# Performance work log

Measured on AMD Instinct MI355X. Metric: run time of the kernel, lower is better.

## Reference

```python
import jax, jax.numpy as jnp
import numpy as np

N_NODES = 32768
N_EDGES = 524288
IN_F = 256
OUT_F = 128
NB = 4


def setup_inputs() -> dict:
    key = jax.random.key(0)
    ks = jax.random.split(key, 12)
    s_in = 1.0 / np.sqrt(IN_F)
    s_out = 1.0 / np.sqrt(OUT_F)
    s_cat = 1.0 / np.sqrt(OUT_F * NB)
    return {
        "x": jax.random.normal(ks[0], (N_NODES, IN_F), dtype=jnp.float32),
        "edge_index": jax.random.randint(ks[1], (2, N_EDGES), 0, N_NODES, dtype=jnp.int64),
        "Wb": jax.random.uniform(ks[2], (NB, IN_F, OUT_F), jnp.float32, -s_in, s_in),
        "bb": jax.random.uniform(ks[3], (NB, OUT_F), jnp.float32, -s_in, s_in),
        "W1": jax.random.uniform(ks[4], (NB, OUT_F, OUT_F), jnp.float32, -s_out, s_out),
        "b1": jax.random.uniform(ks[5], (NB, OUT_F), jnp.float32, -s_out, s_out),
        "W2": jax.random.uniform(ks[6], (NB, OUT_F, OUT_F), jnp.float32, -s_out, s_out),
        "b2": jax.random.uniform(ks[7], (NB, OUT_F), jnp.float32, -s_out, s_out),
        "branch_gates": jnp.ones((NB,), dtype=jnp.float32),
        "temperature": jnp.asarray(1.0, dtype=jnp.float32),
        "Wo": jax.random.uniform(ks[8], (OUT_F * NB, OUT_F), jnp.float32, -s_cat, s_cat),
        "bo": jax.random.uniform(ks[9], (OUT_F,), jnp.float32, -s_cat, s_cat),
    }


def _scatter_mean_step(h, row, col, inv_deg):
    # gather per-edge source features, mean-reduce onto destination nodes
    sums = jax.ops.segment_sum(h[row], col, num_segments=N_NODES)
    return sums * inv_deg


def reference(x, edge_index, Wb, bb, W1, b1, W2, b2, branch_gates, temperature, Wo, bo):
    row, col = edge_index[0], edge_index[1]
    deg = jax.ops.segment_sum(jnp.ones((N_EDGES,), x.dtype), col, num_segments=N_NODES)
    inv_deg = (1.0 / jnp.maximum(deg, 1.0))[:, None]  # empty segments -> 0 (scatter_mean semantics)

    gates = jax.nn.softmax(branch_gates / temperature)

    branch_outputs = []
    for i in range(NB):
        h = x @ Wb[i] + bb[i]                   # [N, OUT_F]
        for _ in range(i):                       # scale = scales[i % 4] = i
            h = _scatter_mean_step(h, row, col, inv_deg)
        h = jax.nn.relu(h @ W1[i] + b1[i]) @ W2[i] + b2[i]
        branch_outputs.append(h * gates[i])

    concat = jnp.concatenate(branch_outputs, axis=1)  # [N, NB*OUT_F]
    return concat @ Wo + bo
```

## Files before the change

### kernel.cpp

```cpp
#include <hip/hip_runtime.h>
#include <math.h>

#define N_NODES 32768
#define N_EDGES 524288
#define IN_F    256
#define OUT_F   128
#define NB      4
#define STRIDE  96

#define NE_BLK   256
#define CONV_BLK 1024
#define GX_BLK   2048
#define GEMM_BLK (N_NODES / 128)
#define M_BLK    (N_NODES / 256)

typedef __attribute__((ext_vector_type(8))) short bf16x8;
typedef __attribute__((ext_vector_type(4))) float f32x4;

__device__ __forceinline__ ushort f2b(float f) {
    uint u = __float_as_uint(f);
    return (ushort)((u + 0x7fffu + ((u >> 16) & 1u)) >> 16);
}
__device__ __forceinline__ float b2f_lo(uint v) { return __uint_as_float(v << 16); }
__device__ __forceinline__ float b2f_hi(uint v) { return __uint_as_float(v & 0xffff0000u); }

__device__ __forceinline__ float softmax_gate(const float* bg, const float* temp, int i) {
    float T = temp[0];
    float mx = fmaxf(fmaxf(bg[0], bg[1]), fmaxf(bg[2], bg[3]));
    float e0 = expf((bg[0] - mx) / T), e1 = expf((bg[1] - mx) / T);
    float e2 = expf((bg[2] - mx) / T), e3 = expf((bg[3] - mx) / T);
    float s = e0 + e1 + e2 + e3;
    float ei = (i == 0) ? e0 : (i == 1) ? e1 : (i == 2) ? e2 : e3;
    return ei / s;
}

__device__ __forceinline__ int detect_i32(const int* __restrict__ ei, int* sflag) {
    if (threadIdx.x < 64) {
        unsigned long long b = __ballot(ei[2 * threadIdx.x + 1] != 0);
        if (threadIdx.x == 0) *sflag = (b != 0ull) ? 1 : 0;
    }
    __syncthreads();
    return *sflag;
}

__global__ __launch_bounds__(256) void fill_all_kernel(
    const int* __restrict__ ei, int* __restrict__ cursor, int* __restrict__ srcs,
    const float* __restrict__ x, ushort* __restrict__ xb,
    const float* __restrict__ Wb, const float* __restrict__ W1,
    const float* __restrict__ W2, const float* __restrict__ Wo,
    const float* __restrict__ bb, const float* __restrict__ b2,
    const float* __restrict__ bo, const float* __restrict__ bg,
    const float* __restrict__ temp,
    ushort* __restrict__ WcT, ushort* __restrict__ WzT,
    float* __restrict__ u, float* __restrict__ cvec) {
    __shared__ float smem[16 * 128];
    __shared__ int sflag;
    int b = blockIdx.x;
    int tid = threadIdx.x;
    if (b < NE_BLK) {
        int i32 = detect_i32(ei, &sflag);
#pragma unroll
        for (int it = 0; it < 8; it++) {
            int e = b * 2048 + it * 256 + tid;
            int r, c;
            if (i32 == 0) { r = ei[2 * e]; c = ei[2 * (N_EDGES + e)]; }
            else          { r = ei[e];     c = ei[N_EDGES + e]; }
            int slot = atomicAdd(&cursor[c], 1);
            if (slot < STRIDE) srcs[(size_t)c * STRIDE + slot] = r;
        }
        return;
    }
    b -= NE_BLK;
    if (b < CONV_BLK) {
#pragma unroll
        for (int it = 0; it < 8; it++) {
            int idx = b * 2048 + it * 256 + tid;
            float4 v = ((const float4*)x)[idx];
            ushort4 o;
            o.x = f2b(v.x); o.y = f2b(v.y); o.z = f2b(v.z); o.w = f2b(v.w);
            ((ushort4*)xb)[idx] = o;
        }
        return;
    }
    b -= CONV_BLK;
    int f = tid & 127, rh = tid >> 7;
    if (b < 64) {
        int i = b >> 4, k0 = (b & 15) * 16;
#pragma unroll
        for (int rr = 0; rr < 8; rr++)
            smem[(rh * 8 + rr) * 128 + f] = Wb[((size_t)i * IN_F + k0 + rh * 8 + rr) * OUT_F + f];
        __syncthreads();
        float acc[8] = {};
        const float* W1i = W1 + (size_t)i * OUT_F * OUT_F;
        for (int j = 0; j < OUT_F; j++) {
            float w1 = W1i[j * OUT_F + f];
#pragma unroll
            for (int rr = 0; rr < 8; rr++) acc[rr] += smem[(rh * 8 + rr) * 128 + j] * w1;
        }
        ushort tmp[8];
#pragma unroll
        for (int rr = 0; rr < 8; rr++) tmp[rr] = f2b(acc[rr]);
        *(uint4*)(WcT + ((size_t)i * OUT_F + f) * IN_F + k0 + rh * 8) = *(uint4*)tmp;
    } else if (b < 96) {
        int id = b - 64;
        int i = id >> 3, j0 = (id & 7) * 16;
#pragma unroll
        for (int rr = 0; rr < 8; rr++)
            smem[(rh * 8 + rr) * 128 + f] = W2[((size_t)i * OUT_F + j0 + rh * 8 + rr) * OUT_F + f];
        __syncthreads();
        float acc[8] = {};
        for (int l = 0; l < OUT_F; l++) {
            float wo = Wo[((size_t)i * OUT_F + l) * OUT_F + f];
#pragma unroll
            for (int rr = 0; rr < 8; rr++) acc[rr] += smem[(rh * 8 + rr) * 128 + l] * wo;
        }
        float g = softmax_gate(bg, temp, i);
        ushort tmp[8];
#pragma unroll
        for (int rr = 0; rr < 8; rr++) tmp[rr] = f2b(g * acc[rr]);
        *(uint4*)(WzT + (size_t)f * (NB * OUT_F) + i * OUT_F + j0 + rh * 8) = *(uint4*)tmp;
    } else {
        int id = b - 96;
        int jc = rh;
        if (id < NB) {
            int i = id;
            float partial = 0.f;
            for (int j = jc * 64; j < jc * 64 + 64; j++)
                partial += bb[i * OUT_F + j] * W1[((size_t)i * OUT_F + j) * OUT_F + f];
            smem[jc * 128 + f] = partial;
            __syncthreads();
            if (jc == 0) u[i * OUT_F + f] = smem[f] + smem[128 + f];
        } else {
            int i = id - NB;
            float partial = 0.f;
            for (int j = jc * 64; j < jc * 64 + 64; j++)
                partial += b2[i * OUT_F + j] * Wo[((size_t)i * OUT_F + j) * OUT_F + f];
            smem[jc * 128 + f] = partial;
            __syncthreads();
            if (jc == 0) {
                float tot = (smem[f] + smem[128 + f]) * softmax_gate(bg, temp, i);
                if (i == 0) tot += bo[f];
                atomicAdd(&cvec[f], tot);
            }
        }
    }
}

#define ACC8(A, V)                                                              \
    A[0] += b2f_lo(V.x); A[1] += b2f_hi(V.x);                                   \
    A[2] += b2f_lo(V.y); A[3] += b2f_hi(V.y);                                   \
    A[4] += b2f_lo(V.z); A[5] += b2f_hi(V.z);                                   \
    A[6] += b2f_lo(V.w); A[7] += b2f_hi(V.w)

#define GATHER_256(INBUF)                                                       \
    float a0[8] = {0.f,0.f,0.f,0.f,0.f,0.f,0.f,0.f};                            \
    float a1[8] = {0.f,0.f,0.f,0.f,0.f,0.f,0.f,0.f};                            \
    int p = s;                                                                  \
    for (; p + 8 <= e; p += 8) {                                                \
        int base = p + 4 * half;                                                \
        int2 s01 = *(const int2*)(srcs + base);                                 \
        int2 s23 = *(const int2*)(srcs + base + 2);                             \
        uint4 v0 = *(const uint4*)(INBUF + (size_t)s01.x * IN_F + fl * 8);      \
        uint4 v1 = *(const uint4*)(INBUF + (size_t)s01.y * IN_F + fl * 8);      \
        uint4 v2 = *(const uint4*)(INBUF + (size_t)s23.x * IN_F + fl * 8);      \
        uint4 v3 = *(const uint4*)(INBUF + (size_t)s23.y * IN_F + fl * 8);      \
        ACC8(a0, v0); ACC8(a1, v1); ACC8(a0, v2); ACC8(a1, v3);                 \
    }                                                                           \
    for (; p + 4 <= e; p += 4) {                                                \
        int2 ss = *(const int2*)(srcs + p + 2 * half);                          \
        uint4 v0 = *(const uint4*)(INBUF + (size_t)ss.x * IN_F + fl * 8);       \
        uint4 v1 = *(const uint4*)(INBUF + (size_t)ss.y * IN_F + fl * 8);       \
        ACC8(a0, v0); ACC8(a1, v1);                                             \
    }                                                                           \
    for (; p + half < e; p += 2) {                                              \
        int src = srcs[p + half];                                               \
        uint4 v0 = *(const uint4*)(INBUF + (size_t)src * IN_F + fl * 8);        \
        ACC8(a0, v0);                                                           \
    }                                                                           \
    _Pragma("unroll") for (int k = 0; k < 8; k++) a0[k] += a1[k];               \
    _Pragma("unroll") for (int k = 0; k < 8; k++) a0[k] += __shfl_down(a0[k], 32);

__global__ __launch_bounds__(256) void prop_x_kernel(
    const ushort* __restrict__ xb, ushort* __restrict__ X1b,
    const int* __restrict__ deg, float* __restrict__ m2,
    const int* __restrict__ srcs) {
    int blk = blockIdx.x;
    int tid = threadIdx.x;
    if (blk >= GX_BLK) {
        int n = (blk - GX_BLK) * 256 + tid;
        int d = deg[n];
        int s = n * STRIDE, e = s + ((d < STRIDE) ? d : STRIDE);
        float sum = 0.f;
        for (int p = s; p < e; ++p) sum += (deg[srcs[p]] > 0) ? 1.0f : 0.0f;
        m2[n] = sum / (float)((d > 1) ? d : 1);
        return;
    }
    int lane = tid & 63;
    int half = lane >> 5, fl = lane & 31;
    for (int i = 0; i < 4; i++) {
        int node = blk * 16 + i * 4 + (tid >> 6);
        int d = deg[node];
        int s = node * STRIDE, e = s + ((d < STRIDE) ? d : STRIDE);
        GATHER_256(xb);
        if (half == 0) {
            float w = 1.0f / (float)((d > 1) ? d : 1);
            uint4 o;
            o.x = (uint)f2b(a0[0] * w) | ((uint)f2b(a0[1] * w) << 16);
            o.y = (uint)f2b(a0[2] * w) | ((uint)f2b(a0[3] * w) << 16);
            o.z = (uint)f2b(a0[4] * w) | ((uint)f2b(a0[5] * w) << 16);
            o.w = (uint)f2b(a0[6] * w) | ((uint)f2b(a0[7] * w) << 16);
            *(uint4*)(X1b + (size_t)node * IN_F + fl * 8) = o;
        }
    }
}

__global__ __launch_bounds__(256) void gemmP_kernel(
    const ushort* __restrict__ xb, const ushort* __restrict__ X1b,
    const ushort* __restrict__ WcT, const float* __restrict__ u,
    const float* __restrict__ b1, const int* __restrict__ deg,
    ushort* __restrict__ R, ushort* __restrict__ PQ) {
    int y = blockIdx.y;
    const ushort* A = (y == 0) ? xb : X1b;
    const ushort* WT = WcT + (size_t)y * OUT_F * IN_F;
    int m0 = blockIdx.x * 128;
    __shared__ ushort As[128][72];
    __shared__ ushort Bs[128][72];
    int tid = threadIdx.x;
    int wv = tid >> 6, lane = tid & 63, quad = lane >> 4, lm = lane & 15;
    f32x4 acc[2][8];
    f32x4 zero = {0.f, 0.f, 0.f, 0.f};
#pragma unroll
    for (int i = 0; i < 2; i++)
#pragma unroll
        for (int j = 0; j < 8; j++) acc[i][j] = zero;
    for (int k0 = 0; k0 < IN_F; k0 += 64) {
        __syncthreads();
#pragma unroll
        for (int it = 0; it < 4; it++) {
            int c = tid + 256 * it;
            int r = c >> 3, c8 = c & 7;
            *(uint4*)&As[r][c8 * 8] = *(const uint4*)(A + (size_t)(m0 + r) * IN_F + k0 + c8 * 8);
            *(uint4*)&Bs[r][c8 * 8] = *(const uint4*)(WT + (size_t)r * IN_F + k0 + c8 * 8);
        }
        __syncthreads();
#pragma unroll
        for (int ks = 0; ks < 2; ks++) {
            bf16x8 af0 = *(const bf16x8*)&As[wv * 32 + lm][ks * 32 + quad * 8];
            bf16x8 af1 = *(const bf16x8*)&As[wv * 32 + 16 + lm][ks * 32 + quad * 8];
#pragma unroll
            for (int nt = 0; nt < 8; nt++) {
                bf16x8 bf = *(const bf16x8*)&Bs[nt * 16 + lm][ks * 32 + quad * 8];
                acc[0][nt] = __builtin_amdgcn_mfma_f32_16x16x32_bf16(af0, bf, acc[0][nt], 0, 0, 0);
                acc[1][nt] = __builtin_amdgcn_mfma_f32_16x16x32_bf16(af1, bf, acc[1][nt], 0, 0, 0);
            }
        }
    }
    if (y >= 2) {
        int pqoff = (y - 2) * OUT_F;
#pragma unroll
        for (int mt = 0; mt < 2; mt++)
#pragma unroll
            for (int r = 0; r < 4; r++) {
                int row = m0 + wv * 32 + mt * 16 + quad * 4 + r;
#pragma unroll
                for (int nt = 0; nt < 8; nt++) {
                    int col = nt * 16 + lm;
                    PQ[(size_t)row * IN_F + pqoff + col] = f2b(acc[mt][nt][r]);
                }
            }
    } else {
        float uv[8], bv[8];
#pragma unroll
        for (int nt = 0; nt < 8; nt++) {
            int col = nt * 16 + lm;
            uv[nt] = u[y * OUT_F + col];
            bv[nt] = b1[y * OUT_F + col];
        }
#pragma unroll
        for (int mt = 0; mt < 2; mt++)
#pragma unroll
            for (int r = 0; r < 4; r++) {
                int row = m0 + wv * 32 + mt * 16 + quad * 4 + r;
                float mval = (y == 0) ? 1.0f : ((deg[row] > 0) ? 1.0f : 0.0f);
#pragma unroll
                for (int nt = 0; nt < 8; nt++) {
                    int col = nt * 16 + lm;
                    float h = acc[mt][nt][r] + mval * uv[nt] + bv[nt];
                    R[(size_t)row * (NB * OUT_F) + y * OUT_F + col] = f2b(fmaxf(h, 0.f));
                }
            }
    }
}

__global__ __launch_bounds__(256) void prop_pq_kernel(
    const ushort* __restrict__ PQ, ushort* __restrict__ R, ushort* __restrict__ Qp,
    const int* __restrict__ deg, const float* __restrict__ m2, float* __restrict__ m3,
    const float* __restrict__ u2, const float* __restrict__ b12,
    const int* __restrict__ srcs) {
    int blk = blockIdx.x;
    int tid = threadIdx.x;
    if (blk >= GX_BLK) {
        int n = (blk - GX_BLK) * 256 + tid;
        int d = deg[n];
        int s = n * STRIDE, e = s + ((d < STRIDE) ? d : STRIDE);
        float sum = 0.f;
        for (int p = s; p < e; ++p) sum += m2[srcs[p]];
        m3[n] = sum / (float)((d > 1) ? d : 1);
        return;
    }
    int lane = tid & 63;
    int half = lane >> 5, fl = lane & 31;
    for (int i = 0; i < 4; i++) {
        int node = blk * 16 + i * 4 + (tid >> 6);
        int d = deg[node];
        int s = node * STRIDE, e = s + ((d < STRIDE) ? d : STRIDE);
        GATHER_256(PQ);
        if (half == 0) {
            float w = 1.0f / (float)((d > 1) ? d : 1);
            if (fl < 16) {
                int col = fl * 8;
                float mv = m2[node];
                float4 ua = *(const float4*)(u2 + col);
                float4 ub = *(const float4*)(u2 + col + 4);
                float4 ba = *(const float4*)(b12 + col);
                float4 bb_ = *(const float4*)(b12 + col + 4);
                float o_[8];
                o_[0] = fmaxf(a0[0] * w + mv * ua.x + ba.x, 0.f);
                o_[1] = fmaxf(a0[1] * w + mv * ua.y + ba.y, 0.f);
                o_[2] = fmaxf(a0[2] * w + mv * ua.z + ba.z, 0.f);
                o_[3] = fmaxf(a0[3] * w + mv * ua.w + ba.w, 0.f);
                o_[4] = fmaxf(a0[4] * w + mv * ub.x + bb_.x, 0.f);
                o_[5] = fmaxf(a0[5] * w + mv * ub.y + bb_.y, 0.f);
                o_[6] = fmaxf(a0[6] * w + mv * ub.z + bb_.z, 0.f);
                o_[7] = fmaxf(a0[7] * w + mv * ub.w + bb_.w, 0.f);
                uint4 o;
                o.x = (uint)f2b(o_[0]) | ((uint)f2b(o_[1]) << 16);
                o.y = (uint)f2b(o_[2]) | ((uint)f2b(o_[3]) << 16);
                o.z = (uint)f2b(o_[4]) | ((uint)f2b(o_[5]) << 16);
                o.w = (uint)f2b(o_[6]) | ((uint)f2b(o_[7]) << 16);
                *(uint4*)(R + (size_t)node * (NB * OUT_F) + 2 * OUT_F + col) = o;
            } else {
                int col = (fl - 16) * 8;
                uint4 o;
                o.x = (uint)f2b(a0[0] * w) | ((uint)f2b(a0[1] * w) << 16);
                o.y = (uint)f2b(a0[2] * w) | ((uint)f2b(a0[3] * w) << 16);
                o.z = (uint)f2b(a0[4] * w) | ((uint)f2b(a0[5] * w) << 16);
                o.w = (uint)f2b(a0[6] * w) | ((uint)f2b(a0[7] * w) << 16);
                *(uint4*)(Qp + (size_t)node * OUT_F + col) = o;
            }
        }
    }
}

__global__ __launch_bounds__(256) void prop_q_kernel(
    const ushort* __restrict__ Qp, ushort* __restrict__ R,
    const int* __restrict__ deg, const float* __restrict__ m3,
    const float* __restrict__ u3, const float* __restrict__ b13,
    const int* __restrict__ srcs) {
    int lane = threadIdx.x & 63;
    int q = lane >> 4, fl = lane & 15;
    for (int i = 0; i < 4; i++) {
        int node = blockIdx.x * 16 + i * 4 + (threadIdx.x >> 6);
        int d = deg[node];
        int s = node * STRIDE, e = s + ((d < STRIDE) ? d : STRIDE);
        float a[8] = {0.f,0.f,0.f,0.f,0.f,0.f,0.f,0.f};
        float b[8] = {0.f,0.f,0.f,0.f,0.f,0.f,0.f,0.f};
        int p = s;
        for (; p + 8 <= e; p += 8) {
            int2 ss = *(const int2*)(srcs + p + 2 * q);
            uint4 v0 = *(const uint4*)(Qp + (size_t)ss.x * OUT_F + fl * 8);
            uint4 v1 = *(const uint4*)(Qp + (size_t)ss.y * OUT_F + fl * 8);
            ACC8(a, v0); ACC8(b, v1);
        }
        for (; p + 4 <= e; p += 4) {
            int src = srcs[p + q];
            uint4 v0 = *(const uint4*)(Qp + (size_t)src * OUT_F + fl * 8);
            ACC8(a, v0);
        }
        if (p + q < e) {
            int src = srcs[p + q];
            uint4 v0 = *(const uint4*)(Qp + (size_t)src * OUT_F + fl * 8);
            ACC8(a, v0);
        }
#pragma unroll
        for (int k = 0; k < 8; k++) a[k] += b[k];
#pragma unroll
        for (int k = 0; k < 8; k++) a[k] += __shfl_down(a[k], 32);
#pragma unroll
        for (int k = 0; k < 8; k++) a[k] += __shfl_down(a[k], 16);
        if (lane < 16) {
            float w = 1.0f / (float)((d > 1) ? d : 1);
            float mv = m3[node];
            int col = fl * 8;
            float4 ua = *(const float4*)(u3 + col);
            float4 ub = *(const float4*)(u3 + col + 4);
            float4 ba = *(const float4*)(b13 + col);
            float4 bb_ = *(const float4*)(b13 + col + 4);
            float o_[8];
            o_[0] = fmaxf(a[0] * w + mv * ua.x + ba.x, 0.f);
            o_[1] = fmaxf(a[1] * w + mv * ua.y + ba.y, 0.f);
            o_[2] = fmaxf(a[2] * w + mv * ua.z + ba.z, 0.f);
            o_[3] = fmaxf(a[3] * w + mv * ua.w + ba.w, 0.f);
            o_[4] = fmaxf(a[4] * w + mv * ub.x + bb_.x, 0.f);
            o_[5] = fmaxf(a[5] * w + mv * ub.y + bb_.y, 0.f);
            o_[6] = fmaxf(a[6] * w + mv * ub.z + bb_.z, 0.f);
            o_[7] = fmaxf(a[7] * w + mv * ub.w + bb_.w, 0.f);
            uint4 o;
            o.x = (uint)f2b(o_[0]) | ((uint)f2b(o_[1]) << 16);
            o.y = (uint)f2b(o_[2]) | ((uint)f2b(o_[3]) << 16);
            o.z = (uint)f2b(o_[4]) | ((uint)f2b(o_[5]) << 16);
            o.w = (uint)f2b(o_[6]) | ((uint)f2b(o_[7]) << 16);
            *(uint4*)(R + (size_t)node * (NB * OUT_F) + 3 * OUT_F + col) = o;
        }
    }
}

__global__ __launch_bounds__(256) void gemm2_mfma_kernel(
    const ushort* __restrict__ R, const ushort* __restrict__ WzT,
    const float* __restrict__ cvec, float* __restrict__ out) {
    int m0 = blockIdx.x * 128;
    const int K = NB * OUT_F;
    __shared__ ushort As[128][72];
    __shared__ ushort Bs[128][72];
    int tid = threadIdx.x;
    int wv = tid >> 6, lane = tid & 63, quad = lane >> 4, lm = lane & 15;
    f32x4 acc[2][8];
    f32x4 zero = {0.f, 0.f, 0.f, 0.f};
#pragma unroll
    for (int i = 0; i < 2; i++)
#pragma unroll
        for (int j = 0; j < 8; j++) acc[i][j] = zero;
    for (int k0 = 0; k0 < K; k0 += 64) {
        __syncthreads();
#pragma unroll
        for (int it = 0; it < 4; it++) {
            int c = tid + 256 * it;
            int r = c >> 3, c8 = c & 7;
            *(uint4*)&As[r][c8 * 8] = *(const uint4*)(R + (size_t)(m0 + r) * K + k0 + c8 * 8);
            *(uint4*)&Bs[r][c8 * 8] = *(const uint4*)(WzT + (size_t)r * K + k0 + c8 * 8);
        }
        __syncthreads();
#pragma unroll
        for (int ks = 0; ks < 2; ks++) {
            bf16x8 af0 = *(const bf16x8*)&As[wv * 32 + lm][ks * 32 + quad * 8];
            bf16x8 af1 = *(const bf16x8*)&As[wv * 32 + 16 + lm][ks * 32 + quad * 8];
#pragma unroll
            for (int nt = 0; nt < 8; nt++) {
                bf16x8 bf = *(const bf16x8*)&Bs[nt * 16 + lm][ks * 32 + quad * 8];
                acc[0][nt] = __builtin_amdgcn_mfma_f32_16x16x32_bf16(af0, bf, acc[0][nt], 0, 0, 0);
                acc[1][nt] = __builtin_amdgcn_mfma_f32_16x16x32_bf16(af1, bf, acc[1][nt], 0, 0, 0);
            }
        }
    }
    float cb[8];
#pragma unroll
    for (int nt = 0; nt < 8; nt++) cb[nt] = cvec[nt * 16 + lm];
#pragma unroll
    for (int mt = 0; mt < 2; mt++)
#pragma unroll
        for (int r = 0; r < 4; r++) {
            int row = m0 + wv * 32 + mt * 16 + quad * 4 + r;
#pragma unroll
            for (int nt = 0; nt < 8; nt++) {
                int col = nt * 16 + lm;
                out[(size_t)row * OUT_F + col] = acc[mt][nt][r] + cb[nt];
            }
        }
}

extern "C" void kernel_launch(void* const* d_in, const int* in_sizes, int n_in,
                              void* d_out, int out_size, void* d_ws, size_t ws_size,
                              hipStream_t stream) {
    const float* x    = (const float*)d_in[0];
    const int*   ei   = (const int*)d_in[1];
    const float* Wb   = (const float*)d_in[2];
    const float* bb   = (const float*)d_in[3];
    const float* W1   = (const float*)d_in[4];
    const float* b1   = (const float*)d_in[5];
    const float* W2   = (const float*)d_in[6];
    const float* b2   = (const float*)d_in[7];
    const float* bg   = (const float*)d_in[8];
    const float* temp = (const float*)d_in[9];
    const float* Wo   = (const float*)d_in[10];
    const float* bo   = (const float*)d_in[11];
    float* out = (float*)d_out;

    char* w = (char*)d_ws;
    size_t used = 0;
    auto alloc = [&](size_t bytes) {
        char* p = w + used;
        used += (bytes + 255) & ~(size_t)255;
        return p;
    };
    int*    cursor = (int*)alloc(N_NODES * 4);
    float*  cvec   = (float*)alloc(OUT_F * 4);
    int*    srcs   = (int*)alloc((size_t)N_NODES * STRIDE * 4);
    float*  m2v    = (float*)alloc(N_NODES * 4);
    float*  m3v    = (float*)alloc(N_NODES * 4);
    float*  u      = (float*)alloc(NB * OUT_F * 4);
    ushort* WcT    = (ushort*)alloc((size_t)NB * IN_F * OUT_F * 2);
    ushort* WzT    = (ushort*)alloc((size_t)NB * OUT_F * OUT_F * 2);
    ushort* xb     = (ushort*)alloc((size_t)N_NODES * IN_F * 2);
    ushort* X1b    = (ushort*)alloc((size_t)N_NODES * IN_F * 2);
    ushort* PQ     = (ushort*)alloc((size_t)N_NODES * IN_F * 2);
    ushort* Qp     = (ushort*)alloc((size_t)N_NODES * OUT_F * 2);
    ushort* R      = (ushort*)alloc((size_t)N_NODES * NB * OUT_F * 2);
    if (used > ws_size) return;

    int* deg = cursor;

    hipMemsetAsync(cursor, 0, N_NODES * 4 + 512, stream);

    fill_all_kernel<<<NE_BLK + CONV_BLK + 104, 256, 0, stream>>>(
        ei, cursor, srcs, x, xb, Wb, W1, W2, Wo, bb, b2, bo, bg, temp, WcT, WzT, u, cvec);

    prop_x_kernel<<<GX_BLK + M_BLK, 256, 0, stream>>>(xb, X1b, deg, m2v, srcs);

    {
        dim3 grid(GEMM_BLK, 4);
        gemmP_kernel<<<grid, 256, 0, stream>>>(xb, X1b, WcT, u, b1, deg, R, PQ);
    }

    prop_pq_kernel<<<GX_BLK + M_BLK, 256, 0, stream>>>(
        PQ, R, Qp, deg, m2v, m3v, u + 2 * OUT_F, b1 + 2 * OUT_F, srcs);

    prop_q_kernel<<<GX_BLK, 256, 0, stream>>>(
        Qp, R, deg, m3v, u + 3 * OUT_F, b1 + 3 * OUT_F, srcs);

    gemm2_mfma_kernel<<<GEMM_BLK, 256, 0, stream>>>(R, WzT, cvec, out);
}
```

Before: 269.2 us.

## Use nontemporal loads/stores, deepen gather unrolling, reorder blocks, add occupancy hints

Switches edge-index loads, the srcs/xb/X1b/PQ/R/Qp/out writes, and the srcs index reads to nontemporal builtins so streaming data bypasses the cache. The gather loops are unrolled further (12 edges per iteration in GATHER_256, 16 in prop_q) to put more loads in flight. The per-node m2/m3 blocks are moved to the front of the grid, and launch_bounds min-blocks hints of 8 are added to the propagation kernels. The risk is that nontemporal stores push out data the following kernel reads straight back (xb, PQ, Qp, R), and that the occupancy hint caps registers and causes spills.

New measurement: 303.8 us. 1.13x slower.

```diff
diff --git a/kernel.cpp b/kernel.cpp
--- a/kernel.cpp
+++ b/kernel.cpp
@@ -16,6 +16,10 @@
 
 typedef __attribute__((ext_vector_type(8))) short bf16x8;
 typedef __attribute__((ext_vector_type(4))) float f32x4;
+typedef __attribute__((ext_vector_type(2))) int    i32x2;
+typedef __attribute__((ext_vector_type(4))) int    i32x4;
+typedef __attribute__((ext_vector_type(4))) uint   u32x4;
+typedef __attribute__((ext_vector_type(4))) ushort u16x4;
 
 __device__ __forceinline__ ushort f2b(float f) {
     uint u = __float_as_uint(f);
@@ -63,10 +67,15 @@
         for (int it = 0; it < 8; it++) {
             int e = b * 2048 + it * 256 + tid;
             int r, c;
-            if (i32 == 0) { r = ei[2 * e]; c = ei[2 * (N_EDGES + e)]; }
-            else          { r = ei[e];     c = ei[N_EDGES + e]; }
+            if (i32 == 0) {
+                r = __builtin_nontemporal_load(ei + 2 * e);
+                c = __builtin_nontemporal_load(ei + 2 * (N_EDGES + e));
+            } else {
+                r = __builtin_nontemporal_load(ei + e);
+                c = __builtin_nontemporal_load(ei + N_EDGES + e);
+            }
             int slot = atomicAdd(&cursor[c], 1);
-            if (slot < STRIDE) srcs[(size_t)c * STRIDE + slot] = r;
+            if (slot < STRIDE) __builtin_nontemporal_store(r, srcs + (size_t)c * STRIDE + slot);
         }
         return;
     }
@@ -75,10 +84,10 @@
 #pragma unroll
         for (int it = 0; it < 8; it++) {
             int idx = b * 2048 + it * 256 + tid;
-            float4 v = ((const float4*)x)[idx];
-            ushort4 o;
+            f32x4 v = __builtin_nontemporal_load((const f32x4*)x + idx);
+            u16x4 o;
             o.x = f2b(v.x); o.y = f2b(v.y); o.z = f2b(v.z); o.w = f2b(v.w);
-            ((ushort4*)xb)[idx] = o;
+            __builtin_nontemporal_store(o, (u16x4*)xb + idx);
         }
         return;
     }
@@ -156,18 +165,22 @@
     float a0[8] = {0.f,0.f,0.f,0.f,0.f,0.f,0.f,0.f};                            \
     float a1[8] = {0.f,0.f,0.f,0.f,0.f,0.f,0.f,0.f};                            \
     int p = s;                                                                  \
-    for (; p + 8 <= e; p += 8) {                                                \
-        int base = p + 4 * half;                                                \
-        int2 s01 = *(const int2*)(srcs + base);                                 \
-        int2 s23 = *(const int2*)(srcs + base + 2);                             \
+    for (; p + 12 <= e; p += 12) {                                              \
+        int base = p + 6 * half;                                                \
+        i32x2 s01 = __builtin_nontemporal_load((const i32x2*)(srcs + base));    \
+        i32x2 s23 = __builtin_nontemporal_load((const i32x2*)(srcs + base + 2));\
+        i32x2 s45 = __builtin_nontemporal_load((const i32x2*)(srcs + base + 4));\
         uint4 v0 = *(const uint4*)(INBUF + (size_t)s01.x * IN_F + fl * 8);      \
         uint4 v1 = *(const uint4*)(INBUF + (size_t)s01.y * IN_F + fl * 8);      \
         uint4 v2 = *(const uint4*)(INBUF + (size_t)s23.x * IN_F + fl * 8);      \
         uint4 v3 = *(const uint4*)(INBUF + (size_t)s23.y * IN_F + fl * 8);      \
-        ACC8(a0, v0); ACC8(a1, v1); ACC8(a0, v2); ACC8(a1, v3);                 \
+        uint4 v4 = *(const uint4*)(INBUF + (size_t)s45.x * IN_F + fl * 8);      \
+        uint4 v5 = *(const uint4*)(INBUF + (size_t)s45.y * IN_F + fl * 8);      \
+        ACC8(a0, v0); ACC8(a1, v1); ACC8(a0, v2);                               \
+        ACC8(a1, v3); ACC8(a0, v4); ACC8(a1, v5);                               \
     }                                                                           \
     for (; p + 4 <= e; p += 4) {                                                \
-        int2 ss = *(const int2*)(srcs + p + 2 * half);                          \
+        i32x2 ss = __builtin_nontemporal_load((const i32x2*)(srcs + p + 2 * half)); \
         uint4 v0 = *(const uint4*)(INBUF + (size_t)ss.x * IN_F + fl * 8);       \
         uint4 v1 = *(const uint4*)(INBUF + (size_t)ss.y * IN_F + fl * 8);       \
         ACC8(a0, v0); ACC8(a1, v1);                                             \
@@ -180,14 +193,14 @@
     _Pragma("unroll") for (int k = 0; k < 8; k++) a0[k] += a1[k];               \
     _Pragma("unroll") for (int k = 0; k < 8; k++) a0[k] += __shfl_down(a0[k], 32);
 
-__global__ __launch_bounds__(256) void prop_x_kernel(
+__global__ __launch_bounds__(256, 8) void prop_x_kernel(
     const ushort* __restrict__ xb, ushort* __restrict__ X1b,
     const int* __restrict__ deg, float* __restrict__ m2,
     const int* __restrict__ srcs) {
     int blk = blockIdx.x;
     int tid = threadIdx.x;
-    if (blk >= GX_BLK) {
-        int n = (blk - GX_BLK) * 256 + tid;
+    if (blk < M_BLK) {
+        int n = blk * 256 + tid;
         int d = deg[n];
         int s = n * STRIDE, e = s + ((d < STRIDE) ? d : STRIDE);
         float sum = 0.f;
@@ -195,6 +208,7 @@
         m2[n] = sum / (float)((d > 1) ? d : 1);
         return;
     }
+    blk -= M_BLK;
     int lane = tid & 63;
     int half = lane >> 5, fl = lane & 31;
     for (int i = 0; i < 4; i++) {
@@ -204,12 +218,12 @@
         GATHER_256(xb);
         if (half == 0) {
             float w = 1.0f / (float)((d > 1) ? d : 1);
-            uint4 o;
+            u32x4 o;
             o.x = (uint)f2b(a0[0] * w) | ((uint)f2b(a0[1] * w) << 16);
             o.y = (uint)f2b(a0[2] * w) | ((uint)f2b(a0[3] * w) << 16);
             o.z = (uint)f2b(a0[4] * w) | ((uint)f2b(a0[5] * w) << 16);
             o.w = (uint)f2b(a0[6] * w) | ((uint)f2b(a0[7] * w) << 16);
-            *(uint4*)(X1b + (size_t)node * IN_F + fl * 8) = o;
+            __builtin_nontemporal_store(o, (u32x4*)(X1b + (size_t)node * IN_F + fl * 8));
         }
     }
 }
@@ -265,7 +279,8 @@
 #pragma unroll
                 for (int nt = 0; nt < 8; nt++) {
                     int col = nt * 16 + lm;
-                    PQ[(size_t)row * IN_F + pqoff + col] = f2b(acc[mt][nt][r]);
+                    __builtin_nontemporal_store(f2b(acc[mt][nt][r]),
+                                                PQ + (size_t)row * IN_F + pqoff + col);
                 }
             }
     } else {
@@ -286,21 +301,22 @@
                 for (int nt = 0; nt < 8; nt++) {
                     int col = nt * 16 + lm;
                     float h = acc[mt][nt][r] + mval * uv[nt] + bv[nt];
-                    R[(size_t)row * (NB * OUT_F) + y * OUT_F + col] = f2b(fmaxf(h, 0.f));
+                    __builtin_nontemporal_store(f2b(fmaxf(h, 0.f)),
+                                                R + (size_t)row * (NB * OUT_F) + y * OUT_F + col);
                 }
             }
     }
 }
 
-__global__ __launch_bounds__(256) void prop_pq_kernel(
+__global__ __launch_bounds__(256, 8) void prop_pq_kernel(
     const ushort* __restrict__ PQ, ushort* __restrict__ R, ushort* __restrict__ Qp,
     const int* __restrict__ deg, const float* __restrict__ m2, float* __restrict__ m3,
     const float* __restrict__ u2, const float* __restrict__ b12,
     const int* __restrict__ srcs) {
     int blk = blockIdx.x;
     int tid = threadIdx.x;
-    if (blk >= GX_BLK) {
-        int n = (blk - GX_BLK) * 256 + tid;
+    if (blk < M_BLK) {
+        int n = blk * 256 + tid;
         int d = deg[n];
         int s = n * STRIDE, e = s + ((d < STRIDE) ? d : STRIDE);
         float sum = 0.f;
@@ -308,6 +324,7 @@
         m3[n] = sum / (float)((d > 1) ? d : 1);
         return;
     }
+    blk -= M_BLK;
     int lane = tid & 63;
     int half = lane >> 5, fl = lane & 31;
     for (int i = 0; i < 4; i++) {
@@ -333,26 +350,26 @@
                 o_[5] = fmaxf(a0[5] * w + mv * ub.y + bb_.y, 0.f);
                 o_[6] = fmaxf(a0[6] * w + mv * ub.z + bb_.z, 0.f);
                 o_[7] = fmaxf(a0[7] * w + mv * ub.w + bb_.w, 0.f);
-                uint4 o;
+                u32x4 o;
                 o.x = (uint)f2b(o_[0]) | ((uint)f2b(o_[1]) << 16);
                 o.y = (uint)f2b(o_[2]) | ((uint)f2b(o_[3]) << 16);
                 o.z = (uint)f2b(o_[4]) | ((uint)f2b(o_[5]) << 16);
                 o.w = (uint)f2b(o_[6]) | ((uint)f2b(o_[7]) << 16);
-                *(uint4*)(R + (size_t)node * (NB * OUT_F) + 2 * OUT_F + col) = o;
+                __builtin_nontemporal_store(o, (u32x4*)(R + (size_t)node * (NB * OUT_F) + 2 * OUT_F + col));
             } else {
                 int col = (fl - 16) * 8;
-                uint4 o;
+                u32x4 o;
                 o.x = (uint)f2b(a0[0] * w) | ((uint)f2b(a0[1] * w) << 16);
                 o.y = (uint)f2b(a0[2] * w) | ((uint)f2b(a0[3] * w) << 16);
                 o.z = (uint)f2b(a0[4] * w) | ((uint)f2b(a0[5] * w) << 16);
                 o.w = (uint)f2b(a0[6] * w) | ((uint)f2b(a0[7] * w) << 16);
-                *(uint4*)(Qp + (size_t)node * OUT_F + col) = o;
-            }
-        }
-    }
-}
-
-__global__ __launch_bounds__(256) void prop_q_kernel(
+                __builtin_nontemporal_store(o, (u32x4*)(Qp + (size_t)node * OUT_F + col));
+            }
+        }
+    }
+}
+
+__global__ __launch_bounds__(256, 8) void prop_q_kernel(
     const ushort* __restrict__ Qp, ushort* __restrict__ R,
     const int* __restrict__ deg, const float* __restrict__ m3,
     const float* __restrict__ u3, const float* __restrict__ b13,
@@ -366,8 +383,16 @@
         float a[8] = {0.f,0.f,0.f,0.f,0.f,0.f,0.f,0.f};
         float b[8] = {0.f,0.f,0.f,0.f,0.f,0.f,0.f,0.f};
         int p = s;
+        for (; p + 16 <= e; p += 16) {
+            i32x4 sq = __builtin_nontemporal_load((const i32x4*)(srcs + p + 4 * q));
+            uint4 v0 = *(const uint4*)(Qp + (size_t)sq.x * OUT_F + fl * 8);
+            uint4 v1 = *(const uint4*)(Qp + (size_t)sq.y * OUT_F + fl * 8);
+            uint4 v2 = *(const uint4*)(Qp + (size_t)sq.z * OUT_F + fl * 8);
+            uint4 v3 = *(const uint4*)(Qp + (size_t)sq.w * OUT_F + fl * 8);
+            ACC8(a, v0); ACC8(b, v1); ACC8(a, v2); ACC8(b, v3);
+        }
         for (; p + 8 <= e; p += 8) {
-            int2 ss = *(const int2*)(srcs + p + 2 * q);
+            i32x2 ss = __builtin_nontemporal_load((const i32x2*)(srcs + p + 2 * q));
             uint4 v0 = *(const uint4*)(Qp + (size_t)ss.x * OUT_F + fl * 8);
             uint4 v1 = *(const uint4*)(Qp + (size_t)ss.y * OUT_F + fl * 8);
             ACC8(a, v0); ACC8(b, v1);
@@ -405,12 +430,12 @@
             o_[5] = fmaxf(a[5] * w + mv * ub.y + bb_.y, 0.f);
             o_[6] = fmaxf(a[6] * w + mv * ub.z + bb_.z, 0.f);
             o_[7] = fmaxf(a[7] * w + mv * ub.w + bb_.w, 0.f);
-            uint4 o;
+            u32x4 o;
             o.x = (uint)f2b(o_[0]) | ((uint)f2b(o_[1]) << 16);
             o.y = (uint)f2b(o_[2]) | ((uint)f2b(o_[3]) << 16);
             o.z = (uint)f2b(o_[4]) | ((uint)f2b(o_[5]) << 16);
             o.w = (uint)f2b(o_[6]) | ((uint)f2b(o_[7]) << 16);
-            *(uint4*)(R + (size_t)node * (NB * OUT_F) + 3 * OUT_F + col) = o;
+            __builtin_nontemporal_store(o, (u32x4*)(R + (size_t)node * (NB * OUT_F) + 3 * OUT_F + col));
         }
     }
 }
@@ -463,7 +488,8 @@
 #pragma unroll
             for (int nt = 0; nt < 8; nt++) {
                 int col = nt * 16 + lm;
-                out[(size_t)row * OUT_F + col] = acc[mt][nt][r] + cb[nt];
+                __builtin_nontemporal_store(acc[mt][nt][r] + cb[nt],
+                                            out + (size_t)row * OUT_F + col);
             }
         }
 }
@@ -514,14 +540,14 @@
     fill_all_kernel<<<NE_BLK + CONV_BLK + 104, 256, 0, stream>>>(
         ei, cursor, srcs, x, xb, Wb, W1, W2, Wo, bb, b2, bo, bg, temp, WcT, WzT, u, cvec);
 
-    prop_x_kernel<<<GX_BLK + M_BLK, 256, 0, stream>>>(xb, X1b, deg, m2v, srcs);
+    prop_x_kernel<<<M_BLK + GX_BLK, 256, 0, stream>>>(xb, X1b, deg, m2v, srcs);
 
     {
         dim3 grid(GEMM_BLK, 4);
         gemmP_kernel<<<grid, 256, 0, stream>>>(xb, X1b, WcT, u, b1, deg, R, PQ);
     }
 
-    prop_pq_kernel<<<GX_BLK + M_BLK, 256, 0, stream>>>(
+    prop_pq_kernel<<<M_BLK + GX_BLK, 256, 0, stream>>>(
         PQ, R, Qp, deg, m2v, m3v, u + 2 * OUT_F, b1 + 2 * OUT_F, srcs);
 
     prop_q_kernel<<<GX_BLK, 256, 0, stream>>>(
```
